# Kernel optimization log

Hardware: AMD Instinct MI355X
Metric: run time of the kernel (lower is better)

Reference implementation:

```python
import jax, jax.numpy as jnp
import numpy as np

N = 50000      # nodes (particles)
E = 1600000    # edges
G = 2000       # graphs (jets)
NEG_SLOPE = 0.2

def setup_inputs() -> dict:
    key = jax.random.key(0)
    ks = jax.random.split(key, 18)
    p = lambda k, s: (jax.random.normal(k, s, jnp.float32) * 0.1)
    return {
        'x': jax.random.normal(ks[0], (N, 3), jnp.float32),
        'edge_index': jax.random.randint(ks[1], (2, E), 0, N, dtype=jnp.int64),
        'batch': jnp.sort(jax.random.randint(ks[2], (N,), 0, G, dtype=jnp.int64)),
        'W1': p(ks[3], (3, 128)),  'a1s': p(ks[4], (4, 32)),  'a1d': p(ks[5], (4, 32)),  'b1': p(ks[6], (128,)),
        'W2': p(ks[7], (128, 128)),'a2s': p(ks[8], (4, 32)),  'a2d': p(ks[9], (4, 32)),  'b2': p(ks[10], (128,)),
        'W3': p(ks[11], (128, 32)),'a3s': p(ks[12], (1, 32)), 'a3d': p(ks[13], (1, 32)), 'b3': p(ks[14], (32,)),
        'Wh': p(ks[15], (32, 2)),  'bh': p(ks[16], (2,)),
    }

def gat_conv(x, src, dst, W, a_src, a_dst, b, concat):
    """PyG GATConv (eval mode): gather-score-softmax-scatter over edges (src->dst)."""
    n = x.shape[0]
    H, C = a_src.shape
    h = (x @ W).reshape(n, H, C)                         # [N,H,C]
    es = jnp.sum(h * a_src, axis=-1)                     # [N,H] source scores
    ed = jnp.sum(h * a_dst, axis=-1)                     # [N,H] dest scores
    e = jax.nn.leaky_relu(es[src] + ed[dst], NEG_SLOPE)  # [E,H]
    # neighbor-wise (per destination node) stable softmax
    m = jax.ops.segment_max(e, dst, num_segments=n)      # [N,H]
    m = jax.lax.stop_gradient(jnp.where(jnp.isfinite(m), m, 0.0))
    w = jnp.exp(e - m[dst])
    z = jax.ops.segment_sum(w, dst, num_segments=n)      # [N,H]
    alpha = w / (z[dst] + 1e-16)                         # [E,H]
    out = jax.ops.segment_sum(h[src] * alpha[:, :, None], dst, num_segments=n)  # [N,H,C]
    out = out.reshape(n, H * C) if concat else out.mean(axis=1)
    return out + b

def reference(x, edge_index, batch, W1, a1s, a1d, b1, W2, a2s, a2d, b2,
              W3, a3s, a3d, b3, Wh, bh):
    n = x.shape[0]
    loops = jnp.arange(n, dtype=edge_index.dtype)        # add_self_loops=True
    src = jnp.concatenate([edge_index[0], loops])
    dst = jnp.concatenate([edge_index[1], loops])
    h = jax.nn.elu(gat_conv(x, src, dst, W1, a1s, a1d, b1, True))
    h = jax.nn.elu(gat_conv(h, src, dst, W2, a2s, a2d, b2, True))
    h = jax.nn.elu(gat_conv(h, src, dst, W3, a3s, a3d, b3, False))
    cnt = jax.ops.segment_sum(jnp.ones((n,), h.dtype), batch, num_segments=G)
    pooled = jax.ops.segment_sum(h, batch, num_segments=G) / jnp.maximum(cnt, 1.0)[:, None]
    return pooled @ Wh + bh                              # [G, n_classes]
```

## Files before the change

kernel.cpp:

```cpp
#include <hip/hip_runtime.h>

#define CAP 80
#define NXCD 8
#define SCAT_BLKS_PER_RANGE 256
#define SCAT_TOTAL (SCAT_BLKS_PER_RANGE*NXCD)

typedef int vint4 __attribute__((ext_vector_type(4)));
__device__ __forceinline__ vint4 ntload_i4(const int* p){ return __builtin_nontemporal_load((const vint4*)p); }

__device__ __forceinline__ float lrelu02(float x){ return x > 0.f ? x : 0.2f*x; }
__device__ __forceinline__ float eluf(float x){ return x > 0.f ? x : (__expf(x)-1.f); }
__device__ __forceinline__ unsigned short f2bf(float x){
  unsigned u = __float_as_uint(x);
  u += 0x7fffu + ((u >> 16) & 1u);
  return (unsigned short)(u >> 16);
}
__device__ __forceinline__ float bf2f(unsigned short b){
  return __uint_as_float(((unsigned)b) << 16);
}

__global__ void scatter_proj1_kernel(const int* __restrict__ src, const int* __restrict__ dst,
                                     int E, int n, int* __restrict__ cnt,
                                     unsigned short* __restrict__ col,
                                     const float* __restrict__ x, const float* __restrict__ W,
                                     const float* __restrict__ as_, const float* __restrict__ ad_,
                                     unsigned short* __restrict__ hout, float* __restrict__ es,
                                     float* __restrict__ ed){
  if (blockIdx.x < SCAT_TOTAL){
    int r  = blockIdx.x & (NXCD-1);
    int bi = blockIdx.x >> 3;
    int lo = (int)((long long)n * r / NXCD);
    int hi = (int)((long long)n * (r+1) / NXCD);
    int stride = SCAT_BLKS_PER_RANGE * 256 * 4;
    for (int e0 = (bi*256 + (int)threadIdx.x)*4; e0 < E; e0 += stride){
      if (e0 + 4 <= E){
        vint4 d4 = ntload_i4(dst + e0);
        vint4 s4 = ntload_i4(src + e0);
        #pragma unroll
        for (int k = 0; k < 4; ++k){
          int d = d4[k];
          if (d >= lo && d < hi){
            int p = atomicAdd(&cnt[d],1);
            if (p < CAP) col[(size_t)d*CAP + p] = (unsigned short)s4[k];
          }
        }
      } else {
        for (int e = e0; e < E; ++e){
          int d = dst[e];
          if (d >= lo && d < hi){
            int p = atomicAdd(&cnt[d],1);
            if (p < CAP) col[(size_t)d*CAP + p] = (unsigned short)src[e];
          }
        }
      }
    }
  } else {
    __shared__ float xs[2][3];
    int node0 = (blockIdx.x - SCAT_TOTAL) * 2;
    int t = threadIdx.x;
    if (t < 6){
      int nn = node0 + t/3;
      xs[t/3][t%3] = (nn < n) ? x[(size_t)nn*3 + t%3] : 0.f;
    }
    __syncthreads();
    int node = node0 + t / 128;
    int o = t % 128;
    if (node >= n) return;
    const float* xr = xs[t / 128];
    float acc = 0.f;
    #pragma unroll
    for (int k = 0; k < 3; ++k) acc = fmaf(xr[k], W[k*128 + o], acc);
    hout[(size_t)node*128 + o] = f2bf(acc);
    float ts = acc * as_[o];
    float td = acc * ad_[o];
    #pragma unroll
    for (int m = 16; m >= 1; m >>= 1){
      ts += __shfl_xor(ts, m);
      td += __shfl_xor(td, m);
    }
    if ((o & 31) == 0){
      es[node*4 + (o>>5)] = ts;
      ed[node*4 + (o>>5)] = td;
    }
  }
}

template<int OUT, int NPT, int H>
__global__ void proj_tiled_kernel(const float* __restrict__ x, const float* __restrict__ W,
                                  const float* __restrict__ as_, const float* __restrict__ ad_,
                                  unsigned short* __restrict__ hout, float* __restrict__ es,
                                  float* __restrict__ ed, int n){
  constexpr int OG = OUT / 4;
  constexpr int NG = 256 / OG;
  constexpr int NODES = NG * NPT;
  __shared__ float xs[128][NODES + 1];
  int node0 = blockIdx.x * NODES;
  int t = threadIdx.x;
  for (int i = t; i < NODES*32; i += 256){
    int nl = i >> 5, kc = i & 31;
    int nn = node0 + nl;
    float4 v = make_float4(0.f,0.f,0.f,0.f);
    if (nn < n) v = *(const float4*)(x + (size_t)nn*128 + kc*4);
    xs[kc*4+0][nl] = v.x;
    xs[kc*4+1][nl] = v.y;
    xs[kc*4+2][nl] = v.z;
    xs[kc*4+3][nl] = v.w;
  }
  __syncthreads();
  int og = t % OG;
  int ng = t / OG;
  float acc[NPT][4];
  #pragma unroll
  for (int p = 0; p < NPT; ++p){ acc[p][0]=0.f; acc[p][1]=0.f; acc[p][2]=0.f; acc[p][3]=0.f; }
  const float* wp = W + og*4;
  #pragma unroll 4
  for (int k = 0; k < 128; ++k){
    float4 w = *(const float4*)(wp + (size_t)k*OUT);
    #pragma unroll
    for (int p = 0; p < NPT; ++p){
      float xv = xs[k][ng*NPT + p];
      acc[p][0] = fmaf(xv, w.x, acc[p][0]);
      acc[p][1] = fmaf(xv, w.y, acc[p][1]);
      acc[p][2] = fmaf(xv, w.z, acc[p][2]);
      acc[p][3] = fmaf(xv, w.w, acc[p][3]);
    }
  }
  int o = og*4;
  float as0 = as_[o], as1 = as_[o+1], as2 = as_[o+2], as3 = as_[o+3];
  float ad0 = ad_[o], ad1 = ad_[o+1], ad2 = ad_[o+2], ad3 = ad_[o+3];
  #pragma unroll
  for (int p = 0; p < NPT; ++p){
    int node = node0 + ng*NPT + p;
    float ts = acc[p][0]*as0 + acc[p][1]*as1 + acc[p][2]*as2 + acc[p][3]*as3;
    float td = acc[p][0]*ad0 + acc[p][1]*ad1 + acc[p][2]*ad2 + acc[p][3]*ad3;
    #pragma unroll
    for (int m = 4; m >= 1; m >>= 1){
      ts += __shfl_xor(ts, m);
      td += __shfl_xor(td, m);
    }
    if (node < n){
      ushort4 hb;
      hb.x = f2bf(acc[p][0]); hb.y = f2bf(acc[p][1]);
      hb.z = f2bf(acc[p][2]); hb.w = f2bf(acc[p][3]);
      *(ushort4*)(hout + (size_t)node*OUT + o) = hb;
      if ((og & 7) == 0){
        int head = og >> 3;
        es[node*H + head] = ts;
        ed[node*H + head] = td;
      }
    }
  }
}

__global__ void agg128_kernel(const unsigned short* __restrict__ h, const float* __restrict__ es,
                              const float* __restrict__ ed, const int* __restrict__ deg,
                              const unsigned short* __restrict__ col, const float* __restrict__ bias,
                              float* __restrict__ out, int n){
  int node = blockIdx.x*4 + (threadIdx.x >> 6);
  int lane = threadIdx.x & 63;
  if (node >= n) return;
  int beg = node*CAP;
  int end = beg + min(deg[node], CAP);
  int head = lane >> 4;
  float ed_h = ed[node*4 + head];
  float a0 = 0.f, a1 = 0.f, z = 0.f;
  int e = beg;
  for (; e + 16 <= end; e += 16){
    uint4 c0 = *(const uint4*)(col + e);
    uint4 c1 = *(const uint4*)(col + e + 8);
    unsigned cw[8] = {c0.x,c0.y,c0.z,c0.w,c1.x,c1.y,c1.z,c1.w};
    int s[16]; float q[16]; unsigned u[16];
    #pragma unroll
    for (int k = 0; k < 8; ++k){ s[2*k] = cw[k] & 0xffffu; s[2*k+1] = cw[k] >> 16; }
    #pragma unroll
    for (int k = 0; k < 16; ++k) q[k] = es[s[k]*4 + head];
    #pragma unroll
    for (int k = 0; k < 16; ++k) u[k] = *(const unsigned*)(h + (size_t)s[k]*128 + 2*lane);
    #pragma unroll
    for (int k = 0; k < 16; ++k){
      float w = __expf(lrelu02(q[k] + ed_h));
      z += w;
      a0 = fmaf(w, __uint_as_float(u[k] << 16), a0);
      a1 = fmaf(w, __uint_as_float(u[k] & 0xffff0000u), a1);
    }
  }
  for (; e + 8 <= end; e += 8){
    uint4 c0 = *(const uint4*)(col + e);
    unsigned cw[4] = {c0.x,c0.y,c0.z,c0.w};
    int s[8]; float q[8]; unsigned u[8];
    #pragma unroll
    for (int k = 0; k < 4; ++k){ s[2*k] = cw[k] & 0xffffu; s[2*k+1] = cw[k] >> 16; }
    #pragma unroll
    for (int k = 0; k < 8; ++k) q[k] = es[s[k]*4 + head];
    #pragma unroll
    for (int k = 0; k < 8; ++k) u[k] = *(const unsigned*)(h + (size_t)s[k]*128 + 2*lane);
    #pragma unroll
    for (int k = 0; k < 8; ++k){
      float w = __expf(lrelu02(q[k] + ed_h));
      z += w;
      a0 = fmaf(w, __uint_as_float(u[k] << 16), a0);
      a1 = fmaf(w, __uint_as_float(u[k] & 0xffff0000u), a1);
    }
  }
  for (; e < end; ++e){
    int s = col[e];
    float w = __expf(lrelu02(es[s*4 + head] + ed_h));
    unsigned u = *(const unsigned*)(h + (size_t)s*128 + 2*lane);
    z += w;
    a0 = fmaf(w, __uint_as_float(u << 16), a0);
    a1 = fmaf(w, __uint_as_float(u & 0xffff0000u), a1);
  }
  {
    float w = __expf(lrelu02(es[node*4 + head] + ed_h));
    unsigned u = *(const unsigned*)(h + (size_t)node*128 + 2*lane);
    z += w;
    a0 = fmaf(w, __uint_as_float(u << 16), a0);
    a1 = fmaf(w, __uint_as_float(u & 0xffff0000u), a1);
  }
  float inv = 1.f / (z + 1e-16f);
  int o = 2*lane;
  float2 r;
  r.x = eluf(a0*inv + bias[o]);
  r.y = eluf(a1*inv + bias[o+1]);
  *(float2*)(out + (size_t)node*128 + o) = r;
}

__global__ void agg32_kernel(const unsigned short* __restrict__ h, const float* __restrict__ es,
                             const float* __restrict__ ed, const int* __restrict__ deg,
                             const unsigned short* __restrict__ col, const float* __restrict__ bias,
                             float* __restrict__ out, int n){
  int node = blockIdx.x*4 + (threadIdx.x >> 6);
  int lane = threadIdx.x & 63;
  if (node >= n) return;
  int beg = node*CAP;
  int end = beg + min(deg[node], CAP);
  int half = lane >> 5;
  int c = lane & 31;
  float ed0 = ed[node];
  float a0 = 0.f, z = 0.f;
  int e = beg;
  for (; e + 16 <= end; e += 16){
    uint4 c0 = *(const uint4*)(col + e + 8*half);
    unsigned cw[4] = {c0.x,c0.y,c0.z,c0.w};
    int s[8]; float q[8], hv[8];
    #pragma unroll
    for (int k = 0; k < 4; ++k){ s[2*k] = cw[k] & 0xffffu; s[2*k+1] = cw[k] >> 16; }
    #pragma unroll
    for (int k = 0; k < 8; ++k) q[k] = es[s[k]];
    #pragma unroll
    for (int k = 0; k < 8; ++k) hv[k] = bf2f(h[(size_t)s[k]*32 + c]);
    #pragma unroll
    for (int k = 0; k < 8; ++k){
      float w = __expf(lrelu02(q[k] + ed0));
      z += w;
      a0 = fmaf(w, hv[k], a0);
    }
  }
  for (; e + 2 <= end; e += 2){
    int s = col[e + half];
    float w = __expf(lrelu02(es[s] + ed0));
    float hv = bf2f(h[(size_t)s*32 + c]);
    z += w;
    a0 = fmaf(w, hv, a0);
  }
  if (e < end && half == 0){
    int s = col[e];
    float w = __expf(lrelu02(es[s] + ed0));
    float hv = bf2f(h[(size_t)s*32 + c]);
    z += w;
    a0 = fmaf(w, hv, a0);
  }
  a0 += __shfl_xor(a0, 32);
  z  += __shfl_xor(z, 32);
  {
    float w = __expf(lrelu02(es[node] + ed0));
    float hv = bf2f(h[(size_t)node*32 + c]);
    z += w;
    a0 = fmaf(w, hv, a0);
  }
  if (half == 0){
    float inv = 1.f / (z + 1e-16f);
    out[(size_t)node*32 + c] = eluf(a0*inv + bias[c]);
  }
}

__global__ void pool_kernel(const float* __restrict__ h3, const int* __restrict__ batch,
                            float* __restrict__ pooled, float* __restrict__ cnt, int n){
  int i = blockIdx.x*blockDim.x + threadIdx.x;
  int node = i >> 5, c = i & 31;
  if (node >= n) return;
  int g = batch[node];
  atomicAdd(&pooled[g*32 + c], h3[(size_t)node*32 + c]);
  if (c == 0) atomicAdd(&cnt[g], 1.f);
}

__global__ void head_kernel(const float* __restrict__ pooled, const float* __restrict__ cnt,
                            const float* __restrict__ Wh, const float* __restrict__ bh,
                            float* __restrict__ out, int G){
  int g = blockIdx.x*blockDim.x + threadIdx.x;
  if (g >= G) return;
  float inv = 1.f / fmaxf(cnt[g], 1.f);
  float o0 = bh[0], o1 = bh[1];
  #pragma unroll
  for (int c = 0; c < 32; ++c){
    float p = pooled[g*32 + c] * inv;
    o0 = fmaf(p, Wh[c*2+0], o0);
    o1 = fmaf(p, Wh[c*2+1], o1);
  }
  out[g*2+0] = o0;
  out[g*2+1] = o1;
}

extern "C" void kernel_launch(void* const* d_in, const int* in_sizes, int n_in,
                              void* d_out, int out_size, void* d_ws, size_t ws_size,
                              hipStream_t stream){
  const float* x   = (const float*)d_in[0];
  const int*   ei  = (const int*)d_in[1];
  const int* batch = (const int*)d_in[2];
  const float* W1  = (const float*)d_in[3];
  const float* a1s = (const float*)d_in[4];
  const float* a1d = (const float*)d_in[5];
  const float* b1  = (const float*)d_in[6];
  const float* W2  = (const float*)d_in[7];
  const float* a2s = (const float*)d_in[8];
  const float* a2d = (const float*)d_in[9];
  const float* b2  = (const float*)d_in[10];
  const float* W3  = (const float*)d_in[11];
  const float* a3s = (const float*)d_in[12];
  const float* a3d = (const float*)d_in[13];
  const float* b3  = (const float*)d_in[14];
  const float* Wh  = (const float*)d_in[15];
  const float* bh  = (const float*)d_in[16];
  const int n = in_sizes[0] / 3;
  const int E = in_sizes[1] / 2;
  const int G = out_size / 2;
  float* out = (float*)d_out;

  char* p = (char*)d_ws;
  auto alloc = [&](size_t bytes)->char*{ char* r = p; p += (bytes + 255) & ~(size_t)255; return r; };
  float* buf_x            = (float*)alloc((size_t)n*128*4);
  unsigned short* buf_h   = (unsigned short*)alloc((size_t)n*128*2);
  float* es     = (float*)alloc((size_t)n*4*4);
  float* ed     = (float*)alloc((size_t)n*4*4);
  float* pooled = (float*)alloc((size_t)G*33*4);
  float* cnt    = pooled + (size_t)G*32;
  int* deg      = (int*)alloc((size_t)n*4);
  unsigned short* col = (unsigned short*)alloc((size_t)n*CAP*2);

  const int* srcr = ei;
  const int* dstr = ei + E;

  hipMemsetAsync(deg, 0, (size_t)n*4, stream);
  hipMemsetAsync(pooled, 0, (size_t)G*33*4, stream);

  int proj_blocks = (n + 1) / 2;
  scatter_proj1_kernel<<<SCAT_TOTAL + proj_blocks, 256, 0, stream>>>(
      srcr, dstr, E, n, deg, col, x, W1, a1s, a1d, buf_h, es, ed);

  agg128_kernel<<<(n+3)/4, 256, 0, stream>>>(buf_h, es, ed, deg, col, b1, buf_x, n);
  proj_tiled_kernel<128,4,4><<<(n+31)/32, 256, 0, stream>>>(buf_x, W2, a2s, a2d, buf_h, es, ed, n);
  agg128_kernel<<<(n+3)/4, 256, 0, stream>>>(buf_h, es, ed, deg, col, b2, buf_x, n);
  proj_tiled_kernel<32,2,1><<<(n+63)/64, 256, 0, stream>>>(buf_x, W3, a3s, a3d, buf_h, es, ed, n);
  agg32_kernel<<<(n+3)/4, 256, 0, stream>>>(buf_h, es, ed, deg, col, b3, buf_x, n);

  pool_kernel<<<((n*32)+255)/256, 256, 0, stream>>>(buf_x, batch, pooled, cnt, n);
  head_kernel<<<(G+255)/256, 256, 0, stream>>>(pooled, cnt, Wh, bh, out, G);
}
```

Before: 350.3 us.

## Replace range-filtered edge scatter with two-pass radix partition by destination range

The old scatter had every block range read the entire edge list eight times and keep only the edges whose destinations fell in its range. Now a first pass reads the edges once and buckets (src,dst) pairs in shared memory into eight destination-range queues, which are appended to global queues. A second kernel scatters each queue into the CSR-like col array, so each XCD touches only its own node range. This cuts the repeated edge reads but adds a global intermediate buffer of 8-byte pairs, an extra launch, and a per-block bucket capacity (QCAPB) that can silently drop edges if one bucket overflows.

Result: slower. 370.6 us (+5.8%).

```diff
diff --git a/kernel.cpp b/kernel.cpp
--- a/kernel.cpp
+++ b/kernel.cpp
@@ -2,6 +2,8 @@
 
 #define CAP 80
 #define NXCD 8
+#define QCAPB 512
+#define CHUNK 2048
 #define SCAT_BLKS_PER_RANGE 256
 #define SCAT_TOTAL (SCAT_BLKS_PER_RANGE*NXCD)
 
@@ -19,44 +21,54 @@
   return __uint_as_float(((unsigned)b) << 16);
 }
 
-__global__ void scatter_proj1_kernel(const int* __restrict__ src, const int* __restrict__ dst,
-                                     int E, int n, int* __restrict__ cnt,
-                                     unsigned short* __restrict__ col,
-                                     const float* __restrict__ x, const float* __restrict__ W,
-                                     const float* __restrict__ as_, const float* __restrict__ ad_,
-                                     unsigned short* __restrict__ hout, float* __restrict__ es,
-                                     float* __restrict__ ed){
-  if (blockIdx.x < SCAT_TOTAL){
-    int r  = blockIdx.x & (NXCD-1);
-    int bi = blockIdx.x >> 3;
-    int lo = (int)((long long)n * r / NXCD);
-    int hi = (int)((long long)n * (r+1) / NXCD);
-    int stride = SCAT_BLKS_PER_RANGE * 256 * 4;
-    for (int e0 = (bi*256 + (int)threadIdx.x)*4; e0 < E; e0 += stride){
-      if (e0 + 4 <= E){
-        vint4 d4 = ntload_i4(dst + e0);
-        vint4 s4 = ntload_i4(src + e0);
-        #pragma unroll
-        for (int k = 0; k < 4; ++k){
-          int d = d4[k];
-          if (d >= lo && d < hi){
-            int p = atomicAdd(&cnt[d],1);
-            if (p < CAP) col[(size_t)d*CAP + p] = (unsigned short)s4[k];
-          }
-        }
-      } else {
-        for (int e = e0; e < E; ++e){
-          int d = dst[e];
-          if (d >= lo && d < hi){
-            int p = atomicAdd(&cnt[d],1);
-            if (p < CAP) col[(size_t)d*CAP + p] = (unsigned short)src[e];
-          }
-        }
+__global__ void radix_proj1_kernel(const int* __restrict__ src, const int* __restrict__ dst,
+                                   int E, int n, int nrb, int qcap,
+                                   int* __restrict__ gcur, int2* __restrict__ qbuf,
+                                   const float* __restrict__ x, const float* __restrict__ W,
+                                   const float* __restrict__ as_, const float* __restrict__ ad_,
+                                   unsigned short* __restrict__ hout, float* __restrict__ es,
+                                   float* __restrict__ ed){
+  if ((int)blockIdx.x < nrb){
+    __shared__ int2 q[NXCD][QCAPB];
+    __shared__ int qc[NXCD];
+    __shared__ int qbase[NXCD];
+    int t = threadIdx.x;
+    if (t < NXCD) qc[t] = 0;
+    __syncthreads();
+    int e0 = blockIdx.x*CHUNK + t*8;
+    if (e0 + 8 <= E){
+      vint4 d40 = ntload_i4(dst + e0), d41 = ntload_i4(dst + e0 + 4);
+      vint4 s40 = ntload_i4(src + e0), s41 = ntload_i4(src + e0 + 4);
+      int dd[8] = {d40[0],d40[1],d40[2],d40[3],d41[0],d41[1],d41[2],d41[3]};
+      int ss[8] = {s40[0],s40[1],s40[2],s40[3],s41[0],s41[1],s41[2],s41[3]};
+      #pragma unroll
+      for (int k = 0; k < 8; ++k){
+        int qi = (int)(((long long)dd[k] * NXCD) / n);
+        int pos = atomicAdd(&qc[qi], 1);
+        if (pos < QCAPB) q[qi][pos] = make_int2(ss[k], dd[k]);
       }
+    } else {
+      for (int e = e0; e < E; ++e){
+        int d = dst[e];
+        int qi = (int)(((long long)d * NXCD) / n);
+        int pos = atomicAdd(&qc[qi], 1);
+        if (pos < QCAPB) q[qi][pos] = make_int2(src[e], d);
+      }
+    }
+    __syncthreads();
+    if (t < NXCD) qbase[t] = atomicAdd(&gcur[t], min(qc[t], QCAPB));
+    __syncthreads();
+    #pragma unroll
+    for (int qi = 0; qi < NXCD; ++qi){
+      int cq = min(qc[qi], QCAPB);
+      int2* gq = qbuf + (size_t)qi*qcap;
+      int b0 = qbase[qi];
+      for (int i = t; i < cq; i += 256)
+        if (b0 + i < qcap) gq[b0 + i] = q[qi][i];
     }
   } else {
     __shared__ float xs[2][3];
-    int node0 = (blockIdx.x - SCAT_TOTAL) * 2;
+    int node0 = ((int)blockIdx.x - nrb) * 2;
     int t = threadIdx.x;
     if (t < 6){
       int nn = node0 + t/3;
@@ -81,6 +93,28 @@
     if ((o & 31) == 0){
       es[node*4 + (o>>5)] = ts;
       ed[node*4 + (o>>5)] = td;
+    }
+  }
+}
+
+__global__ void scatter_q_kernel(const int2* __restrict__ qbuf, const int* __restrict__ gcur,
+                                 int qcap, int* __restrict__ cnt, unsigned short* __restrict__ col){
+  int r  = blockIdx.x & (NXCD-1);
+  int bi = blockIdx.x >> 3;
+  int len = min(gcur[r], qcap);
+  const int2* qb = qbuf + (size_t)r*qcap;
+  int stride = SCAT_BLKS_PER_RANGE * 256 * 2;
+  for (int i0 = (bi*256 + (int)threadIdx.x)*2; i0 < len; i0 += stride){
+    if (i0 + 2 <= len){
+      vint4 e2 = ntload_i4((const int*)(qb + i0));
+      int p0 = atomicAdd(&cnt[e2[1]], 1);
+      int p1 = atomicAdd(&cnt[e2[3]], 1);
+      if (p0 < CAP) col[(size_t)e2[1]*CAP + p0] = (unsigned short)e2[0];
+      if (p1 < CAP) col[(size_t)e2[3]*CAP + p1] = (unsigned short)e2[2];
+    } else {
+      int2 e = qb[i0];
+      int p = atomicAdd(&cnt[e.y], 1);
+      if (p < CAP) col[(size_t)e.y*CAP + p] = (unsigned short)e.x;
     }
   }
 }
@@ -335,6 +369,7 @@
   const int E = in_sizes[1] / 2;
   const int G = out_size / 2;
   float* out = (float*)d_out;
+  const int qcap = (E / NXCD) * 5 / 4 + 1024;
 
   char* p = (char*)d_ws;
   auto alloc = [&](size_t bytes)->char*{ char* r = p; p += (bytes + 255) & ~(size_t)255; return r; };
@@ -346,16 +381,21 @@
   float* cnt    = pooled + (size_t)G*32;
   int* deg      = (int*)alloc((size_t)n*4);
   unsigned short* col = (unsigned short*)alloc((size_t)n*CAP*2);
+  int* gcur     = (int*)alloc(NXCD*4);
+  int2* qbuf    = (int2*)alloc((size_t)NXCD*qcap*8);
 
   const int* srcr = ei;
   const int* dstr = ei + E;
 
   hipMemsetAsync(deg, 0, (size_t)n*4, stream);
+  hipMemsetAsync(gcur, 0, NXCD*4, stream);
   hipMemsetAsync(pooled, 0, (size_t)G*33*4, stream);
 
+  int nrb = (E + CHUNK - 1) / CHUNK;
   int proj_blocks = (n + 1) / 2;
-  scatter_proj1_kernel<<<SCAT_TOTAL + proj_blocks, 256, 0, stream>>>(
-      srcr, dstr, E, n, deg, col, x, W1, a1s, a1d, buf_h, es, ed);
+  radix_proj1_kernel<<<nrb + proj_blocks, 256, 0, stream>>>(
+      srcr, dstr, E, n, nrb, qcap, gcur, qbuf, x, W1, a1s, a1d, buf_h, es, ed);
+  scatter_q_kernel<<<SCAT_TOTAL, 256, 0, stream>>>(qbuf, gcur, qcap, deg, col);
 
   agg128_kernel<<<(n+3)/4, 256, 0, stream>>>(buf_h, es, ed, deg, col, b1, buf_x, n);
   proj_tiled_kernel<128,4,4><<<(n+31)/32, 256, 0, stream>>>(buf_x, W2, a2s, a2d, buf_h, es, ed, n);
```
